# Kernel tuning notes

Measured on AMD Instinct MI355X. Metric: run time of the kernel, lower is better.

Reference implementation:

```python
import jax, jax.numpy as jnp
import numpy as np

HIDDEN = 1024
ATT_FEAT = 2048
EMBED = 512


def setup_inputs() -> dict:
    key = jax.random.key(0)
    k1, k2, k3, k4, k5, k6 = jax.random.split(key, 6)
    B, S, N = 16, 64, 196
    hidden = jax.random.normal(k1, (B, S, HIDDEN), dtype=jnp.float32)
    feats = jax.random.normal(k2, (B, N, ATT_FEAT), dtype=jnp.float32)
    att_mask = jax.random.randint(k3, (B, N), 0, 2, dtype=jnp.int32)
    # parameters (scaled like default torch Linear init)
    w_h = jax.random.normal(k4, (HIDDEN, EMBED), dtype=jnp.float32) / np.sqrt(HIDDEN)
    w_u = jax.random.normal(k5, (ATT_FEAT, EMBED), dtype=jnp.float32) / np.sqrt(ATT_FEAT)
    b = jnp.ones((EMBED,), dtype=jnp.float32)
    w = jax.random.normal(k6, (EMBED,), dtype=jnp.float32) / np.sqrt(EMBED)
    return {"hidden": hidden, "feats": feats, "att_mask": att_mask,
            "w_h": w_h, "w_u": w_u, "b": b, "w": w}


def reference(hidden, feats, att_mask, w_h, w_u, b, w):
    # hidden: [B,S,H], feats: [B,N,F], att_mask: [B,N]
    Wh = jnp.einsum('bsh,he->bse', hidden, w_h)          # [B,S,E]
    Uv = jnp.einsum('bnf,fe->bne', feats, w_u)           # [B,N,E] (feats repeat is redundant; same math)
    # additive attention energies: tanh(Wh + Uv + b) . w  -> [B,S,N]
    e = jnp.tanh(Wh[:, :, None, :] + Uv[:, None, :, :] + b)
    scores = jnp.einsum('bsne,e->bsn', e, w)             # [B,S,N]
    scores = jnp.where(att_mask[:, None, :] == 0, jnp.float32(-1e9), scores)
    weights = jax.nn.softmax(scores, axis=-1)            # [B,S,N]
    attn_feats = jnp.einsum('bsn,bnf->bsf', weights, feats)  # [B,S,F]
    return attn_feats, weights
```

## Files before the change

### kernel.cpp

```cpp
#include <hip/hip_runtime.h>
#include <math.h>

#define BATCH 16
#define SEQ 64
#define NKEY 196
#define NPAD 224
#define HIDDEN 1024
#define ATT_FEAT 2048
#define EMBED 512
#define MPAD 3200

using half8    = __attribute__((ext_vector_type(8))) _Float16;
using half4    = __attribute__((ext_vector_type(4))) _Float16;
using f32x4    = __attribute__((ext_vector_type(4))) float;
using f32x16   = __attribute__((ext_vector_type(16))) float;
using float4v  = __attribute__((ext_vector_type(4))) float;

#define KCONST (-2.8853900817779268f)
#define LOG2E  (1.4426950408889634f)

__device__ __forceinline__ void gl_lds16(const _Float16* g, _Float16* l) {
    __builtin_amdgcn_global_load_lds(
        (const __attribute__((address_space(1))) unsigned int*)g,
        (__attribute__((address_space(3))) unsigned int*)l, 16, 0, 0);
}

__device__ inline void prep_a128(
    const float* __restrict__ A, _Float16* __restrict__ T,
    int K, int Mreal, int tm, int tk, int t)
{
    const int r  = t >> 1;
    const int hf = t & 1;
    const int grow = tm * 128 + r;
    float f[32];
    if (grow < Mreal) {
        const float* src = A + (size_t)grow * K + tk * 64 + hf * 32;
        #pragma unroll
        for (int q = 0; q < 8; ++q) {
            float4v v = *(const float4v*)(src + q * 4);
            f[q*4+0] = v.x; f[q*4+1] = v.y; f[q*4+2] = v.z; f[q*4+3] = v.w;
        }
    } else {
        #pragma unroll
        for (int j = 0; j < 32; ++j) f[j] = 0.f;
    }
    const int tkk = tk * 2 + hf;
    const size_t base = ((size_t)tm * (K >> 5) + tkk) * 4096;
    #pragma unroll
    for (int s = 0; s < 2; ++s)
        #pragma unroll
        for (int kh = 0; kh < 2; ++kh) {
            half8 h;
            #pragma unroll
            for (int j = 0; j < 8; ++j)
                h[j] = (_Float16)f[s * 16 + kh * 8 + j];
            *(half8*)(T + base + (size_t)((s * 2 + kh) * 128 + r) * 8) = h;
        }
}

__device__ inline void prep_b128(
    const float* __restrict__ W, _Float16* __restrict__ T,
    int K, int N, int tn, int tk, int t, float (*tile)[129])
{
    {
        const int kr = t >> 2;
        const int nc = (t & 3) * 32;
        const float* src = W + (size_t)(tk * 64 + kr) * N + tn * 128 + nc;
        #pragma unroll
        for (int q = 0; q < 8; ++q) {
            float4v v = *(const float4v*)(src + q * 4);
            tile[kr][nc + q*4 + 0] = v.x; tile[kr][nc + q*4 + 1] = v.y;
            tile[kr][nc + q*4 + 2] = v.z; tile[kr][nc + q*4 + 3] = v.w;
        }
    }
    __syncthreads();
    {
        const int c  = t >> 1;
        const int hf = t & 1;
        const int tkk = tk * 2 + hf;
        const size_t base = ((size_t)tn * (K >> 5) + tkk) * 4096;
        #pragma unroll
        for (int s = 0; s < 2; ++s)
            #pragma unroll
            for (int kh = 0; kh < 2; ++kh) {
                half8 h;
                #pragma unroll
                for (int j = 0; j < 8; ++j)
                    h[j] = (_Float16)tile[hf * 32 + s * 16 + kh * 8 + j][c];
                *(half8*)(T + base + (size_t)((s * 2 + kh) * 128 + c) * 8) = h;
            }
    }
}

__device__ inline void prep_bT(
    const float* __restrict__ Wb, _Float16* __restrict__ T,
    int tn, int tk, int t, float (*tile)[129])
{
    {
        const int kr = t >> 2;
        const int nc = (t & 3) * 32;
        const int gn = tk * 64 + kr;
        #pragma unroll
        for (int q = 0; q < 8; ++q) {
            float4v v = {0.f, 0.f, 0.f, 0.f};
            if (gn < NKEY)
                v = *(const float4v*)(Wb + (size_t)gn * ATT_FEAT + tn * 128 + nc + q * 4);
            tile[kr][nc + q*4 + 0] = v.x; tile[kr][nc + q*4 + 1] = v.y;
            tile[kr][nc + q*4 + 2] = v.z; tile[kr][nc + q*4 + 3] = v.w;
        }
    }
    __syncthreads();
    {
        const int c  = t >> 1;
        const int hf = t & 1;
        const int tkk = tk * 2 + hf;
        if (tkk < 7) {
            const size_t base = ((size_t)tn * 7 + tkk) * 4096;
            #pragma unroll
            for (int s = 0; s < 2; ++s)
                #pragma unroll
                for (int kh = 0; kh < 2; ++kh) {
                    half8 h;
                    #pragma unroll
                    for (int j = 0; j < 8; ++j)
                        h[j] = (_Float16)tile[hf * 32 + s * 16 + kh * 8 + j][c];
                    *(half8*)(T + base + (size_t)((s * 2 + kh) * 128 + c) * 8) = h;
                }
        }
    }
}

__global__ __launch_bounds__(256) void uber_prep(
    const float* __restrict__ hidden, const float* __restrict__ feats,
    const float* __restrict__ w_h, const float* __restrict__ w_u,
    _Float16* HA, _Float16* FA, _Float16* HB, _Float16* UB, _Float16* FT)
{
    __shared__ float tile[64][129];
    const int id = blockIdx.x;
    const int t  = threadIdx.x;
    if (id < 128) {
        prep_a128(hidden, HA, HIDDEN, BATCH * SEQ, id >> 4, id & 15, t);
    } else if (id < 928) {
        const int j = id - 128;
        prep_a128(feats, FA, ATT_FEAT, BATCH * NKEY, j >> 5, j & 31, t);
    } else if (id < 992) {
        const int j = id - 928;
        prep_b128(w_h, HB, HIDDEN, EMBED, j >> 4, j & 15, t, tile);
    } else if (id < 1120) {
        const int j = id - 992;
        prep_b128(w_u, UB, ATT_FEAT, EMBED, j >> 5, j & 31, t, tile);
    } else {
        const int j = id - 1120;
        const int b = j >> 6, rem = j & 63;
        prep_bT(feats + (size_t)b * NKEY * ATT_FEAT,
                FT + (size_t)b * 16 * 7 * 4096, rem >> 2, rem & 3, t, tile);
    }
}

__global__ __launch_bounds__(256) void uber_gemm(
    const _Float16* __restrict__ HA, const _Float16* __restrict__ HB,
    const _Float16* __restrict__ FA, const _Float16* __restrict__ UB,
    const float* __restrict__ bvec, _Float16* __restrict__ WhP,
    _Float16* __restrict__ UvP)
{
    __shared__ __align__(16) _Float16 L[2][3][4096];

    const int hh = blockIdx.x;
    const int t0 = (hh & 7) * 58 + (hh >> 3);

    const _Float16 *Aimg, *Bimg;
    const float* bias = nullptr;
    _Float16* C;
    int rt, ct, tk0, aK;
    if (t0 < 400) {
        const int ks = t0 / 100, rem = t0 % 100;
        rt = rem >> 2; ct = rem & 3;
        Aimg = FA; Bimg = UB;
        aK = ATT_FEAT >> 5; tk0 = ks * 16;
        C = UvP + (size_t)ks * MPAD * EMBED;
        if (ks == 0) bias = bvec;
    } else {
        const int v = t0 - 400;
        const int ks = v >> 5, rem = v & 31;
        rt = rem >> 2; ct = rem & 3;
        Aimg = HA; Bimg = HB;
        aK = HIDDEN >> 5; tk0 = ks * 16;
        C = WhP + (size_t)ks * (BATCH * SEQ) * EMBED;
    }

    const int tid = threadIdx.x, lane = tid & 63, w = tid >> 6;
    const int wr = w >> 1, wc = w & 1;
    const int l31 = lane & 31, kh = lane >> 5;

    const int isB = w >> 1;
    const int whf = w & 1;
    const _Float16* srcMat = isB ? Bimg : Aimg;
    const int majorTile = isB ? ct : rt;
    const _Float16* src0 =
        srcMat + ((size_t)majorTile * aK + tk0) * 4096 + whf * 2048 + lane * 8;

    f32x16 acc[2][2] = {};

    auto stage = [&](int buf, int t) {
        const _Float16* s = src0 + (size_t)t * 4096;
        _Float16* d = &L[isB][buf][0] + whf * 2048 + lane * 8;
        #pragma unroll
        for (int c = 0; c < 4; ++c)
            gl_lds16(s + c * 512, d + c * 512);
    };

    auto compute = [&](int buf) {
        #pragma unroll
        for (int s = 0; s < 2; ++s) {
            const int rb = (s * 2 + kh) * 128;
            half8 a[2], b[2];
            #pragma unroll
            for (int m = 0; m < 2; ++m)
                a[m] = *(const half8*)&L[0][buf][(rb + wr * 64 + m * 32 + l31) * 8];
            #pragma unroll
            for (int n = 0; n < 2; ++n)
                b[n] = *(const half8*)&L[1][buf][(rb + wc * 64 + n * 32 + l31) * 8];
            __builtin_amdgcn_s_setprio(1);
            #pragma unroll
            for (int m = 0; m < 2; ++m)
                #pragma unroll
                for (int n = 0; n < 2; ++n)
                    acc[m][n] = __builtin_amdgcn_mfma_f32_32x32x16_f16(a[m], b[n], acc[m][n], 0, 0, 0);
            __builtin_amdgcn_s_setprio(0);
        }
    };

    stage(0, 0); stage(1, 1);
    int cur = 0, nxt = 2;
    #pragma unroll 1
    for (int t = 0; t < 16; ++t) {
        if (t + 1 < 16) asm volatile("s_waitcnt vmcnt(4)" ::: "memory");
        else            asm volatile("s_waitcnt vmcnt(0)" ::: "memory");
        __builtin_amdgcn_s_barrier();
        if (t + 2 < 16) stage(nxt, t + 2);
        __builtin_amdgcn_sched_barrier(0);
        compute(cur);
        __builtin_amdgcn_sched_barrier(0);
        cur = (cur == 2) ? 0 : cur + 1;
        nxt = (nxt == 2) ? 0 : nxt + 1;
    }

    #pragma unroll
    for (int m = 0; m < 2; ++m) {
        const int row0 = rt * 128 + wr * 64 + m * 32;
        #pragma unroll
        for (int n = 0; n < 2; ++n) {
            const int colg = ct * 128 + wc * 64 + n * 32 + l31;
            const float bv = bias ? bias[colg] : 0.f;
            #pragma unroll
            for (int r = 0; r < 16; ++r) {
                const int row = (r & 3) + 8 * (r >> 2) + 4 * kh;
                C[(size_t)(row0 + row) * EMBED + colg] =
                    (_Float16)((acc[m][n][r] + bv) * KCONST);
            }
        }
    }
}

__global__ __launch_bounds__(256) void scores4_kernel(
    const _Float16* __restrict__ WhP, const _Float16* __restrict__ UvP,
    const float* __restrict__ wvec, float* __restrict__ scr4)
{
    const int n0 = blockIdx.x * 16;
    const int eq = blockIdx.y;
    const int b  = blockIdx.z;
    const int tid = threadIdx.x;
    const int w    = tid >> 6;
    const int lane = tid & 63;

    __shared__ float whs[64 * 64];
    __shared__ float uvs[16][64];

    const size_t WHS = (size_t)(BATCH * SEQ) * EMBED;
    const size_t UVS = (size_t)MPAD * EMBED;

    float acc[4] = {};
    char* whsB = (char*)whs;

    for (int ch = 0; ch < 2; ++ch) {
        const int e0 = eq * 128 + ch * 64;
        {
            const int r = tid >> 2;
            const _Float16* Wr = WhP + (size_t)(b * SEQ + r) * EMBED + e0 + (tid & 3) * 16;
            half8 h0 = *(const half8*)(Wr);
            half8 h1 = *(const half8*)(Wr + 8);
            half8 g0 = *(const half8*)(Wr + WHS);
            half8 g1 = *(const half8*)(Wr + WHS + 8);
            float f[16];
            #pragma unroll
            for (int j = 0; j < 8; ++j) {
                f[j]     = (float)h0[j] + (float)g0[j];
                f[8 + j] = (float)h1[j] + (float)g1[j];
            }
            #pragma unroll
            for (int q = 0; q < 4; ++q) {
                const int cc = (tid & 3) * 16 + q * 4;
                float4v v = { f[q*4+0], f[q*4+1], f[q*4+2], f[q*4+3] };
                *(float4v*)(whsB + r * 256 + ((cc * 4) ^ ((r & 15) << 4))) = v;
            }
        }
        {
            const int nl = tid >> 4;
            const int c4 = tid & 15;
            const int nr = (n0 + nl < NKEY) ? (n0 + nl) : (NKEY - 1);
            const _Float16* Ur = UvP + (size_t)(b * NKEY + nr) * EMBED + e0 + c4 * 4;
            half4 u0 = *(const half4*)(Ur);
            half4 u1 = *(const half4*)(Ur + UVS);
            half4 u2 = *(const half4*)(Ur + 2 * UVS);
            half4 u3 = *(const half4*)(Ur + 3 * UVS);
            float4v u;
            u.x = ((float)u0[0] + (float)u1[0]) + ((float)u2[0] + (float)u3[0]);
            u.y = ((float)u0[1] + (float)u1[1]) + ((float)u2[1] + (float)u3[1]);
            u.z = ((float)u0[2] + (float)u1[2]) + ((float)u2[2] + (float)u3[2]);
            u.w = ((float)u0[3] + (float)u1[3]) + ((float)u2[3] + (float)u3[3]);
            *(float4v*)&uvs[nl][c4 * 4] = u;
        }
        __syncthreads();

        #pragma unroll
        for (int ec = 0; ec < 8; ++ec) {
            const int sb = lane * 256;
            float4v wh0 = *(const float4v*)(whsB + sb + ((ec * 32 +  0) ^ ((lane & 15) << 4)));
            float4v wh1 = *(const float4v*)(whsB + sb + ((ec * 32 + 16) ^ ((lane & 15) << 4)));
            float wf[8];
            #pragma unroll
            for (int i = 0; i < 8; ++i) wf[i] = wvec[e0 + ec * 8 + i];
            #pragma unroll
            for (int j = 0; j < 4; ++j) {
                const int nl = w * 4 + j;
                float4v u0 = *(const float4v*)&uvs[nl][ec * 8];
                float4v u1 = *(const float4v*)&uvs[nl][ec * 8 + 4];
                float t0 = __builtin_amdgcn_exp2f(wh0.x + u0.x);
                float t1 = __builtin_amdgcn_exp2f(wh0.y + u0.y);
                float t2 = __builtin_amdgcn_exp2f(wh0.z + u0.z);
                float t3 = __builtin_amdgcn_exp2f(wh0.w + u0.w);
                float t4 = __builtin_amdgcn_exp2f(wh1.x + u1.x);
                float t5 = __builtin_amdgcn_exp2f(wh1.y + u1.y);
                float t6 = __builtin_amdgcn_exp2f(wh1.z + u1.z);
                float t7 = __builtin_amdgcn_exp2f(wh1.w + u1.w);
                float a = acc[j];
                a = fmaf(wf[0], __builtin_amdgcn_rcpf(1.f + t0), a);
                a = fmaf(wf[1], __builtin_amdgcn_rcpf(1.f + t1), a);
                a = fmaf(wf[2], __builtin_amdgcn_rcpf(1.f + t2), a);
                a = fmaf(wf[3], __builtin_amdgcn_rcpf(1.f + t3), a);
                a = fmaf(wf[4], __builtin_amdgcn_rcpf(1.f + t4), a);
                a = fmaf(wf[5], __builtin_amdgcn_rcpf(1.f + t5), a);
                a = fmaf(wf[6], __builtin_amdgcn_rcpf(1.f + t6), a);
                a = fmaf(wf[7], __builtin_amdgcn_rcpf(1.f + t7), a);
                acc[j] = a;
            }
        }
        __syncthreads();
    }

    float* dst = scr4 + ((size_t)eq * (BATCH * SEQ) + b * SEQ + lane) * NKEY;
    #pragma unroll
    for (int j = 0; j < 4; ++j) {
        const int n = n0 + w * 4 + j;
        if (n < NKEY) dst[n] = 2.f * acc[j];
    }
}

__global__ __launch_bounds__(256) void attn_mfma(
    const float* __restrict__ scr4, const int* __restrict__ mask,
    const _Float16* __restrict__ FT,
    float* __restrict__ weights_out, float* __restrict__ out)
{
    const int fb = blockIdx.x;
    const int b  = blockIdx.y;
    const int t  = threadIdx.x;
    const int lane = t & 63, w = t >> 6;
    const int wr = w >> 1, wc = w & 1;
    const int l31 = lane & 31, khl = lane >> 5;

    __shared__ __align__(16) _Float16 wtL[7 * 4 * 64 * 8];
    __shared__ __align__(16) _Float16 Lb[3][4096];

    const _Float16* FTb = FT + (size_t)b * 16 * 7 * 4096 + (size_t)fb * 7 * 4096;

    auto stage = [&](int buf, int kt) {
        const _Float16* s = FTb + (size_t)kt * 4096 + w * 1024 + lane * 8;
        _Float16* d = &Lb[buf][0] + w * 1024 + lane * 8;
        gl_lds16(s, d);
        gl_lds16(s + 512, d + 512);
    };

    stage(0, 0); stage(1, 1);

    #pragma unroll
    for (int i = 0; i < 7; ++i)
        *(half8*)&wtL[(i * 256 + t) * 8] = (half8)(_Float16)0.f;

    asm volatile("s_waitcnt lgkmcnt(0)" ::: "memory");
    __builtin_amdgcn_s_barrier();

    {
        const int r  = t >> 2;
        const int ln = t & 3;
        const size_t SCRS = (size_t)(BATCH * SEQ) * NKEY;
        const float* p = scr4 + (size_t)(b * SEQ + r) * NKEY;
        const int* mrow = mask + b * NKEY;
        float v[49];
        float mx = -INFINITY;
        #pragma unroll
        for (int j = 0; j < 49; ++j) {
            const int n = ln + 4 * j;
            float s = (p[n] + p[SCRS + n]) + (p[2 * SCRS + n] + p[3 * SCRS + n]);
            if (mrow[n] == 0) s = -1e9f;
            v[j] = s;
            mx = fmaxf(mx, s);
        }
        mx = fmaxf(mx, __shfl_xor(mx, 1));
        mx = fmaxf(mx, __shfl_xor(mx, 2));
        float sum = 0.f;
        #pragma unroll
        for (int j = 0; j < 49; ++j) {
            v[j] = __builtin_amdgcn_exp2f((v[j] - mx) * LOG2E);
            sum += v[j];
        }
        sum += __shfl_xor(sum, 1);
        sum += __shfl_xor(sum, 2);
        const float inv = __builtin_amdgcn_rcpf(sum);
        float* wrow = weights_out + (size_t)(b * SEQ + r) * NKEY;
        #pragma unroll
        for (int j = 0; j < 49; ++j) {
            const int n = ln + 4 * j;
            const float wv = v[j] * inv;
            if (fb == 0) wrow[n] = wv;
            const int grp = ((n >> 4) & 1) * 2 + ((n >> 3) & 1);
            wtL[(((n >> 5) * 4 + grp) * 64 + r) * 8 + (n & 7)] = (_Float16)wv;
        }
    }
    asm volatile("s_waitcnt lgkmcnt(0)" ::: "memory");

    f32x16 acc[2] = {};
    #pragma unroll 1
    for (int kt = 0; kt < 7; ++kt) {
        if (kt < 6) asm volatile("s_waitcnt vmcnt(2)" ::: "memory");
        else        asm volatile("s_waitcnt vmcnt(0)" ::: "memory");
        __builtin_amdgcn_s_barrier();
        if (kt + 2 < 7) stage((kt + 2) % 3, kt + 2);
        __builtin_amdgcn_sched_barrier(0);
        const int buf = kt % 3;
        #pragma unroll
        for (int ks = 0; ks < 2; ++ks) {
            half8 a = *(const half8*)&wtL[(((kt * 4) + ks * 2 + khl) * 64 + wr * 32 + l31) * 8];
            half8 b0 = *(const half8*)&Lb[buf][((ks * 2 + khl) * 128 + wc * 64 + l31) * 8];
            half8 b1 = *(const half8*)&Lb[buf][((ks * 2 + khl) * 128 + wc * 64 + 32 + l31) * 8];
            acc[0] = __builtin_amdgcn_mfma_f32_32x32x16_f16(a, b0, acc[0], 0, 0, 0);
            acc[1] = __builtin_amdgcn_mfma_f32_32x32x16_f16(a, b1, acc[1], 0, 0, 0);
        }
        __builtin_amdgcn_sched_barrier(0);
    }

    #pragma unroll
    for (int nf = 0; nf < 2; ++nf) {
        const int f = fb * 128 + wc * 64 + nf * 32 + l31;
        #pragma unroll
        for (int r = 0; r < 16; ++r) {
            const int srow = wr * 32 + (r & 3) + 8 * (r >> 2) + 4 * khl;
            out[(size_t)(b * SEQ + srow) * ATT_FEAT + f] = acc[nf][r];
        }
    }
}

extern "C" void kernel_launch(void* const* d_in, const int* in_sizes, int n_in,
                              void* d_out, int out_size, void* d_ws, size_t ws_size,
                              hipStream_t stream)
{
    const float* hidden = (const float*)d_in[0];
    const float* feats  = (const float*)d_in[1];
    const int*   mask   = (const int*)  d_in[2];
    const float* w_h    = (const float*)d_in[3];
    const float* w_u    = (const float*)d_in[4];
    const float* bvec   = (const float*)d_in[5];
    const float* wvec   = (const float*)d_in[6];

    float* out         = (float*)d_out;
    float* attn_out    = out;
    float* weights_out = out + (size_t)BATCH * SEQ * ATT_FEAT;

    _Float16* WhP = (_Float16*)d_ws;
    _Float16* UvP = WhP + (size_t)2 * BATCH * SEQ * EMBED;
    float*    scr4 = (float*)(UvP + (size_t)4 * MPAD * EMBED);
    _Float16* FA = (_Float16*)(scr4 + (size_t)4 * BATCH * SEQ * NKEY);
    _Float16* HA = FA + (size_t)MPAD * ATT_FEAT;
    _Float16* UB = HA + (size_t)BATCH * SEQ * HIDDEN;
    _Float16* HB = UB + (size_t)EMBED * ATT_FEAT;
    _Float16* FT = HB + (size_t)EMBED * HIDDEN;

    uber_prep<<<dim3(2144), 256, 0, stream>>>(
        hidden, feats, w_h, w_u, HA, FA, HB, UB, FT);

    uber_gemm<<<dim3(464), 256, 0, stream>>>(
        HA, HB, FA, UB, bvec, WhP, UvP);

    scores4_kernel<<<dim3((NKEY + 15) / 16, 4, BATCH), 256, 0, stream>>>(
        WhP, UvP, wvec, scr4);

    attn_mfma<<<dim3(16, 16), 256, 0, stream>>>(
        scr4, mask, FT, weights_out, attn_out);
}
```

Baseline: 84.80 us.

## Move feats transpose prep from prep kernel into scores kernel blocks

The transposed fp16 feats image (FT) was built in uber_prep before the GEMM, even though only the final attention kernel needs it. That work now runs as extra blocks of the scores kernel, which shares its LDS buffer with the scores path. This shortens the prep kernel on the critical path before the GEMM and lets the transpose run alongside the scores computation. The cost is a larger, mixed-workload scores launch with a bigger shared-memory footprint per block.

```diff
diff --git a/kernel.cpp b/kernel.cpp
--- a/kernel.cpp
+++ b/kernel.cpp
@@ -133,7 +133,7 @@
 __global__ __launch_bounds__(256) void uber_prep(
     const float* __restrict__ hidden, const float* __restrict__ feats,
     const float* __restrict__ w_h, const float* __restrict__ w_u,
-    _Float16* HA, _Float16* FA, _Float16* HB, _Float16* UB, _Float16* FT)
+    _Float16* HA, _Float16* FA, _Float16* HB, _Float16* UB)
 {
     __shared__ float tile[64][129];
     const int id = blockIdx.x;
@@ -146,14 +146,9 @@
     } else if (id < 992) {
         const int j = id - 928;
         prep_b128(w_h, HB, HIDDEN, EMBED, j >> 4, j & 15, t, tile);
-    } else if (id < 1120) {
+    } else {
         const int j = id - 992;
         prep_b128(w_u, UB, ATT_FEAT, EMBED, j >> 5, j & 31, t, tile);
-    } else {
-        const int j = id - 1120;
-        const int b = j >> 6, rem = j & 63;
-        prep_bT(feats + (size_t)b * NKEY * ATT_FEAT,
-                FT + (size_t)b * 16 * 7 * 4096, rem >> 2, rem & 3, t, tile);
     }
 }
 
@@ -262,19 +257,32 @@
     }
 }
 
-__global__ __launch_bounds__(256) void scores4_kernel(
+__global__ __launch_bounds__(256) void scores_ft(
     const _Float16* __restrict__ WhP, const _Float16* __restrict__ UvP,
-    const float* __restrict__ wvec, float* __restrict__ scr4)
-{
-    const int n0 = blockIdx.x * 16;
-    const int eq = blockIdx.y;
-    const int b  = blockIdx.z;
+    const float* __restrict__ wvec, const float* __restrict__ feats,
+    float* __restrict__ scr4, _Float16* __restrict__ FT)
+{
+    __shared__ __align__(16) char smem[64 * 129 * 4];
+    const int id = blockIdx.x;
     const int tid = threadIdx.x;
+
+    if (id >= 832) {
+        const int j = id - 832;
+        const int b = j >> 6, rem = j & 63;
+        prep_bT(feats + (size_t)b * NKEY * ATT_FEAT,
+                FT + (size_t)b * 16 * 7 * 4096, rem >> 2, rem & 3, tid,
+                (float(*)[129])smem);
+        return;
+    }
+
+    const int n0 = (id % 13) * 16;
+    const int eq = (id / 13) & 3;
+    const int b  = id / 52;
     const int w    = tid >> 6;
     const int lane = tid & 63;
 
-    __shared__ float whs[64 * 64];
-    __shared__ float uvs[16][64];
+    float* whs = (float*)smem;
+    float (*uvs)[64] = (float(*)[64])(smem + 16384);
 
     const size_t WHS = (size_t)(BATCH * SEQ) * EMBED;
     const size_t UVS = (size_t)MPAD * EMBED;
@@ -494,14 +502,14 @@
     _Float16* HB = UB + (size_t)EMBED * ATT_FEAT;
     _Float16* FT = HB + (size_t)EMBED * HIDDEN;
 
-    uber_prep<<<dim3(2144), 256, 0, stream>>>(
-        hidden, feats, w_h, w_u, HA, FA, HB, UB, FT);
+    uber_prep<<<dim3(1120), 256, 0, stream>>>(
+        hidden, feats, w_h, w_u, HA, FA, HB, UB);
 
     uber_gemm<<<dim3(464), 256, 0, stream>>>(
         HA, HB, FA, UB, bvec, WhP, UvP);
 
-    scores4_kernel<<<dim3((NKEY + 15) / 16, 4, BATCH), 256, 0, stream>>>(
-        WhP, UvP, wvec, scr4);
+    scores_ft<<<dim3(1856), 256, 0, stream>>>(
+        WhP, UvP, wvec, feats, scr4, FT);
 
     attn_mfma<<<dim3(16, 16), 256, 0, stream>>>(
         scr4, mask, FT, weights_out, attn_out);
```

Result: faster. 77.27 us (-8.9%).
